# Optimization experiments

Hardware: AMD Instinct MI355X
Metric: run time of the kernel (lower is better)

## Reference

```python
import jax, jax.numpy as jnp
import numpy as np

N, E = 20000, 4096
IN_DIM, DET_DIM, HID, OUT = 512, 256, 256, 2
HALF = HID // 2
EPS = 1e-6


def setup_inputs() -> dict:
    key = jax.random.key(0)
    ks = jax.random.split(key, 20)
    g = lambda k, shape, fan_in: jax.random.normal(k, shape, jnp.float32) / np.sqrt(fan_in)
    return {
        "x": jax.random.normal(ks[0], (N, IN_DIM), jnp.float32),
        "z": jax.random.normal(ks[1], (N, DET_DIM), jnp.float32),
        "incidence": jax.random.uniform(ks[2], (N, E), jnp.float32),
        "edge_weights": jax.random.uniform(ks[3], (E,), jnp.float32),
        "psi_w": g(ks[4], (IN_DIM, HALF), IN_DIM), "psi_b": jnp.zeros((HALF,), jnp.float32),
        "phi_w": g(ks[5], (DET_DIM, HALF), DET_DIM), "phi_b": jnp.zeros((HALF,), jnp.float32),
        "g1_w": g(ks[6], (2 * HALF, HID), 2 * HALF), "g1_b": jnp.zeros((HID,), jnp.float32),
        "g2_w": g(ks[7], (HID, HALF), HID), "g2_b": jnp.zeros((HALF,), jnp.float32),
        "th1": g(ks[8], (HALF, HID), HALF), "b1": jnp.zeros((HID,), jnp.float32),
        "th2": g(ks[9], (HID, HID), HID), "b2": jnp.zeros((HID,), jnp.float32),
        "out_w": g(ks[10], (HID, OUT), HID), "out_b": jnp.zeros((OUT,), jnp.float32),
    }


def hconv(X, H, w, theta, bias):
    # HGNN-style message passing: Dv^{-1/2} H W De^{-1} H^T Dv^{-1/2} (X theta) + b
    Xt = X @ theta                              # [N,F]
    De = H.sum(axis=0)                          # [E] edge degree
    Dv = H @ w                                  # [N] weighted node degree
    inv_sqrt_dv = jax.lax.rsqrt(jnp.maximum(Dv, EPS))[:, None]
    He = H.T @ (Xt * inv_sqrt_dv)               # [E,F] gather to hyperedges
    He = He * (w / jnp.maximum(De, EPS))[:, None]
    return (H @ He) * inv_sqrt_dv + bias        # scatter back to nodes


def reference(x, z, incidence, edge_weights,
              psi_w, psi_b, phi_w, phi_b,
              g1_w, g1_b, g2_w, g2_b,
              th1, b1, th2, b2, out_w, out_b):
    proj_x = x @ psi_w + psi_b                  # [N,HALF]
    proj_z = z @ phi_w + phi_b                  # [N,HALF]
    cat = jnp.concatenate([proj_x, proj_z], axis=1)
    gate = jax.nn.sigmoid(jax.nn.relu(cat @ g1_w + g1_b) @ g2_w + g2_b)
    fused = gate * proj_z + (1.0 - gate) * proj_x
    h = jax.nn.relu(hconv(fused, incidence, edge_weights, th1, b1))
    h = jax.nn.relu(hconv(h, incidence, edge_weights, th2, b2))
    logits = h @ out_w + out_b                  # [N,OUT]
    return logits, gate
```

## Files before the change

kernel.cpp:

```cpp
#include <hip/hip_runtime.h>
#include <hip/hip_bf16.h>


typedef __bf16 bf16_t;
typedef __attribute__((ext_vector_type(8))) __bf16 bf16x8;
typedef __attribute__((ext_vector_type(4))) __bf16 bf16x4;
typedef __attribute__((ext_vector_type(4))) float f32x4;

#define NN 20000
#define NE 4096
#define NNP 20480
#define AT_S 16
#define NEB 8
#define NNB 160

__device__ __forceinline__ f32x4 mfma16(bf16x8 a, bf16x8 b, f32x4 c) {
  return __builtin_amdgcn_mfma_f32_16x16x32_bf16(a, b, c, 0, 0, 0);
}

__device__ __forceinline__ void stats_body(int vbx, int vby,
    const float* __restrict__ H, const float* __restrict__ w,
    float* __restrict__ Dvp, float* __restrict__ Dep, bf16_t* __restrict__ Hbp,
    float (*dvl)[17], float (*deP)[512]) {
  int t = threadIdx.x, l = t & 63, wv = t >> 6;
  long e0 = (long)vbx * 512;
  long n0 = (long)vby * 128;
  long pA = ((e0 >> 6) + (l >> 4)) * (long)NNP;
  long pB = pA + 4 * (long)NNP;
  int inner = (l & 15) * 4;
  f32x4 wa = *(const f32x4*)(w + e0 + l * 4);
  f32x4 wb = *(const f32x4*)(w + e0 + 256 + l * 4);
  f32x4 dea; dea[0] = dea[1] = dea[2] = dea[3] = 0.f;
  f32x4 deb; deb[0] = deb[1] = deb[2] = deb[3] = 0.f;
  #pragma unroll 4
  for (int i = 0; i < 32; ++i) {
    long row = n0 + wv * 32 + i;
    float s;
    if (row < NN) {
      f32x4 ua = *(const f32x4*)(H + row * NE + e0 + l * 4);
      f32x4 ub = *(const f32x4*)(H + row * NE + e0 + 256 + l * 4);
      bf16x4 pa, pb;
      #pragma unroll
      for (int j = 0; j < 4; ++j) { pa[j] = (__bf16)ua[j]; pb[j] = (__bf16)ub[j]; }
      *(bf16x4*)(Hbp + (pA + row) * 64 + inner) = pa;
      *(bf16x4*)(Hbp + (pB + row) * 64 + inner) = pb;
      dea += ua; deb += ub;
      s = ua[0]*wa[0] + ua[1]*wa[1] + ua[2]*wa[2] + ua[3]*wa[3]
        + ub[0]*wb[0] + ub[1]*wb[1] + ub[2]*wb[2] + ub[3]*wb[3];
    } else {
      bf16x4 z;
      #pragma unroll
      for (int j = 0; j < 4; ++j) z[j] = (__bf16)0.f;
      *(bf16x4*)(Hbp + (pA + row) * 64 + inner) = z;
      *(bf16x4*)(Hbp + (pB + row) * 64 + inner) = z;
      s = 0.f;
    }
    s += __shfl_xor(s, 1);
    s += __shfl_xor(s, 2);
    if ((l & 3) == 0) dvl[wv * 32 + i][l >> 2] = s;
  }
  *(f32x4*)(&deP[wv][l * 4]) = dea;
  *(f32x4*)(&deP[wv][256 + l * 4]) = deb;
  __syncthreads();
  if (t < 128) {
    float s = 0.f;
    #pragma unroll
    for (int j = 0; j < 16; ++j) s += dvl[t][j];
    Dvp[(long)vbx * NNP + n0 + t] = s;
  }
  {
    float s0 = deP[0][t] + deP[1][t] + deP[2][t] + deP[3][t];
    float s1 = deP[0][256 + t] + deP[1][256 + t] + deP[2][256 + t] + deP[3][256 + t];
    Dep[(long)vby * NE + e0 + t] = s0;
    Dep[(long)vby * NE + e0 + 256 + t] = s1;
  }
}

__device__ __forceinline__ void cat_gemm_body(const float* __restrict__ Av, int lda,
    const bf16_t* __restrict__ Bt, int K, const float* __restrict__ bias,
    bf16_t* __restrict__ dst, int vbx) {
  int tid = threadIdx.x, l = tid & 63, wv = tid >> 6;
  int lr = l & 15, lq = l >> 4;
  int mo = vbx * 32 + (wv >> 1) * 16;
  int no = (wv & 1) * 64;
  f32x4 acc[4] = {};
  for (int k0 = 0; k0 < K; k0 += 32) {
    int row = mo + lr;
    bf16x8 a;
    if (row < NN) {
      const float* ap = Av + (long)row * lda + k0 + lq * 8;
      f32x4 u0 = *(const f32x4*)ap, u1 = *(const f32x4*)(ap + 4);
      #pragma unroll
      for (int j = 0; j < 4; ++j) { a[j] = (__bf16)u0[j]; a[j + 4] = (__bf16)u1[j]; }
    } else {
      #pragma unroll
      for (int j = 0; j < 8; ++j) a[j] = (__bf16)0.f;
    }
    #pragma unroll
    for (int ni = 0; ni < 4; ++ni) {
      bf16x8 b = *(const bf16x8*)(Bt + (long)(no + ni * 16 + lr) * K + k0 + lq * 8);
      acc[ni] = mfma16(a, b, acc[ni]);
    }
  }
  #pragma unroll
  for (int ni = 0; ni < 4; ++ni) {
    int colf = no + ni * 16 + lr;
    int rb = mo + lq * 4;
    float bs = bias[colf];
    #pragma unroll
    for (int r = 0; r < 4; ++r) {
      int n = rb + r;
      if (n < NN) dst[(long)n * 256 + colf] = (__bf16)(acc[ni][r] + bs);
    }
  }
}

__global__ __launch_bounds__(256) void fusedA_kern(const float* __restrict__ H,
    const float* __restrict__ w, float* __restrict__ Dvp, float* __restrict__ Dep,
    bf16_t* __restrict__ Hbp,
    const float* __restrict__ x, const bf16_t* __restrict__ psi_wt,
    const float* __restrict__ psi_b,
    const float* __restrict__ z, const bf16_t* __restrict__ phi_wt,
    const float* __restrict__ phi_b, bf16_t* __restrict__ cat) {
  __shared__ float dvl[128][17];
  __shared__ float deP[4][512];
  int bid = blockIdx.x;
  if (bid < 1280) {
    stats_body(bid & 7, bid >> 3, H, w, Dvp, Dep, Hbp, dvl, deP);
  } else if (bid < 1905) {
    cat_gemm_body(x, 512, psi_wt, 512, psi_b, cat, bid - 1280);
  } else {
    cat_gemm_body(z, 256, phi_wt, 256, phi_b, cat + 128, bid - 1905);
  }
}

__global__ __launch_bounds__(256) void fusedB_kern(const float* __restrict__ Dvp,
    const float* __restrict__ Dep, const float* __restrict__ w,
    float* __restrict__ isd, float* __restrict__ es,
    const bf16_t* __restrict__ cat, const bf16_t* __restrict__ g1w,
    const float* __restrict__ g1b, bf16_t* __restrict__ hid1) {
  int bid = blockIdx.x;
  if (bid < 79) {
    int t = bid * 256 + threadIdx.x;
    if (t < NN) {
      float s = 0.f;
      #pragma unroll
      for (int b = 0; b < NEB; ++b) s += Dvp[(long)b * NNP + t];
      isd[t] = rsqrtf(fmaxf(s, 1e-6f));
    }
    if (t < NE) {
      float s = 0.f;
      #pragma unroll 8
      for (int b = 0; b < NNB; ++b) s += Dep[(long)b * NE + t];
      es[t] = w[t] / fmaxf(s, 1e-6f);
    }
    return;
  }
  int i = bid - 79;
  int vbx = i % 625, vby = i / 625;
  int tid = threadIdx.x, l = tid & 63, wv = tid >> 6;
  int lr = l & 15, lq = l >> 4;
  int mo = vbx * 32 + (wv >> 1) * 16;
  int no = vby * 128 + (wv & 1) * 64;
  f32x4 acc[4] = {};
  for (int k0 = 0; k0 < 256; k0 += 32) {
    int row = mo + lr;
    bf16x8 a;
    if (row < NN) {
      a = *(const bf16x8*)(cat + (long)row * 256 + k0 + lq * 8);
    } else {
      #pragma unroll
      for (int j = 0; j < 8; ++j) a[j] = (__bf16)0.f;
    }
    #pragma unroll
    for (int ni = 0; ni < 4; ++ni) {
      bf16x8 b = *(const bf16x8*)(g1w + (long)(no + ni * 16 + lr) * 256 + k0 + lq * 8);
      acc[ni] = mfma16(a, b, acc[ni]);
    }
  }
  #pragma unroll
  for (int ni = 0; ni < 4; ++ni) {
    int colf = no + ni * 16 + lr;
    int rb = mo + lq * 4;
    float bs = g1b[colf];
    #pragma unroll
    for (int r = 0; r < 4; ++r) {
      int n = rb + r;
      if (n < NN) {
        float xx = acc[ni][r] + bs;
        hid1[(long)n * 256 + colf] = (__bf16)(xx > 0.f ? xx : 0.f);
      }
    }
  }
}

__global__ void cvtw_kern(const float* __restrict__ psi, const float* __restrict__ phi,
                          const float* __restrict__ g1,  const float* __restrict__ g2,
                          const float* __restrict__ th1, const float* __restrict__ th2,
                          bf16_t* dpsi, bf16_t* dphi, bf16_t* dg1, bf16_t* dg2,
                          bf16_t* dth1, bf16_t* dth2) {
  int t = blockIdx.x * 256 + threadIdx.x;
  if (t < 65536) {
    int nc = t >> 9, k = t & 511; dpsi[t] = (__bf16)psi[k * 128 + nc];
  } else if (t < 98304) {
    int i = t - 65536; int nc = i >> 8, k = i & 255; dphi[i] = (__bf16)phi[k * 128 + nc];
  } else if (t < 163840) {
    int i = t - 98304; int nc = i >> 8, k = i & 255; dg1[i] = (__bf16)g1[k * 256 + nc];
  } else if (t < 196608) {
    int i = t - 163840; int nc = i >> 8, k = i & 255; dg2[i] = (__bf16)g2[k * 128 + nc];
  } else if (t < 229376) {
    int i = t - 196608; int nc = i >> 7, k = i & 127; dth1[i] = (__bf16)th1[k * 256 + nc];
  } else if (t < 294912) {
    int i = t - 229376; int nc = i >> 8, k = i & 255; dth2[i] = (__bf16)th2[k * 256 + nc];
  }
}

__global__ __launch_bounds__(256) void gate_y_kern(
    const bf16_t* __restrict__ hid1, const bf16_t* __restrict__ g2w,
    const float* __restrict__ g2b, const bf16_t* __restrict__ cat,
    const bf16_t* __restrict__ th1w, const float* __restrict__ isd,
    float* __restrict__ gate_out, bf16_t* __restrict__ Yf) {
  __shared__ bf16_t fl[32 * 132];
  int t = threadIdx.x, l = t & 63, wv = t >> 6;
  int lr = l & 15, lq = l >> 4;
  if (blockIdx.x >= 625) {
    bf16x8 z;
    #pragma unroll
    for (int j = 0; j < 8; ++j) z[j] = (__bf16)0.f;
    #pragma unroll
    for (int i = 0; i < 4; ++i)
      *(bf16x8*)(Yf + (((long)(wv + i * 4) * 640 + blockIdx.x) * 64 + l) * 8) = z;
    return;
  }
  long n0 = (long)blockIdx.x * 32;
  int hm = wv >> 1, nq = wv & 1;
  int mo = hm * 16, no = nq * 64;
  f32x4 acc[4] = {};
  for (int k0 = 0; k0 < 256; k0 += 32) {
    bf16x8 a = *(const bf16x8*)(hid1 + (n0 + mo + lr) * 256 + k0 + lq * 8);
    #pragma unroll
    for (int ni = 0; ni < 4; ++ni) {
      bf16x8 b = *(const bf16x8*)(g2w + (long)(no + ni * 16 + lr) * 256 + k0 + lq * 8);
      acc[ni] = mfma16(a, b, acc[ni]);
    }
  }
  #pragma unroll
  for (int ni = 0; ni < 4; ++ni) {
    int colf = no + ni * 16 + lr;
    float bs = g2b[colf];
    #pragma unroll
    for (int r = 0; r < 4; ++r) {
      long n = n0 + mo + lq * 4 + r;
      float g = 1.f / (1.f + __expf(-(acc[ni][r] + bs)));
      gate_out[n * 128 + colf] = g;
      float px = (float)cat[n * 256 + colf];
      float pz = (float)cat[n * 256 + 128 + colf];
      fl[(mo + lq * 4 + r) * 132 + colf] = (__bf16)(g * pz + (1.f - g) * px);
    }
  }
  __syncthreads();
  int hm2 = wv >> 1, f128 = (wv & 1) * 128;
  f32x4 acc2[8] = {};
  for (int k0 = 0; k0 < 128; k0 += 32) {
    bf16x8 a = *(const bf16x8*)(fl + (hm2 * 16 + lr) * 132 + k0 + lq * 8);
    #pragma unroll
    for (int ni = 0; ni < 8; ++ni) {
      bf16x8 b = *(const bf16x8*)(th1w + (long)(f128 + ni * 16 + lr) * 128 + k0 + lq * 8);
      acc2[ni] = mfma16(a, b, acc2[ni]);
    }
  }
  int lanep = (hm2 * 2 + (lq >> 1)) * 16 + lr;
  #pragma unroll
  for (int ni = 0; ni < 8; ++ni) {
    int fblk = (f128 >> 4) + ni;
    bf16x4 pk;
    #pragma unroll
    for (int r = 0; r < 4; ++r) {
      long n = n0 + hm2 * 16 + lq * 4 + r;
      pk[r] = (__bf16)(acc2[ni][r] * isd[n]);
    }
    *(bf16x4*)(Yf + (((long)fblk * 640 + blockIdx.x) * 64 + lanep) * 8 + (lq & 1) * 4) = pk;
  }
}

__global__ __launch_bounds__(512) void at_gemm_kern(const bf16_t* __restrict__ Hbp,
                                                    const bf16_t* __restrict__ Yf,
                                                    bf16_t* __restrict__ part) {
  __shared__ bf16_t T[2][128 * 72];
  int t = threadIdx.x, l = t & 63, wv = t >> 6;
  int lr = l & 15, lq = l >> 4;
  int eh = wv >> 2, fq = wv & 3;
  int e0 = blockIdx.x * 128;
  int s0 = blockIdx.y * 20;
  int rp = t >> 4;
  int ck = t & 15;
  f32x4 acc[4][4] = {};
  const bf16_t* src = Hbp + (((long)(e0 >> 6) + (ck >> 3)) * NNP + (long)s0 * 64 + 2 * rp) * 64
                          + (ck & 7) * 8;
  bf16x8 ra = *(const bf16x8*)src;
  bf16x8 rb = *(const bf16x8*)(src + 64);
  {
    #pragma unroll
    for (int j = 0; j < 8; ++j) {
      int jj = (j + ck) & 7;
      int el = ck * 8 + jj;
      unsigned lo = (unsigned)__builtin_bit_cast(unsigned short, (__bf16)ra[jj]);
      unsigned hi = (unsigned)__builtin_bit_cast(unsigned short, (__bf16)rb[jj]);
      *(unsigned*)(&T[0][el * 72 + rp * 2]) = lo | (hi << 16);
    }
    src += 64 * 64;
    ra = *(const bf16x8*)src;
    rb = *(const bf16x8*)(src + 64);
  }
  for (int i = 0; i < 20; ++i) {
    __syncthreads();
    if (i + 1 < 20) {
      int nb = (i + 1) & 1;
      #pragma unroll
      for (int j = 0; j < 8; ++j) {
        int jj = (j + ck) & 7;
        int el = ck * 8 + jj;
        unsigned lo = (unsigned)__builtin_bit_cast(unsigned short, (__bf16)ra[jj]);
        unsigned hi = (unsigned)__builtin_bit_cast(unsigned short, (__bf16)rb[jj]);
        *(unsigned*)(&T[nb][el * 72 + rp * 2]) = lo | (hi << 16);
      }
    }
    if (i + 2 < 20) {
      src += 64 * 64;
      ra = *(const bf16x8*)src;
      rb = *(const bf16x8*)(src + 64);
    }
    int cb = i & 1;
    int s = s0 + i;
    #pragma unroll
    for (int k32 = 0; k32 < 2; ++k32) {
      bf16x8 a[4], b[4];
      #pragma unroll
      for (int ni = 0; ni < 4; ++ni)
        a[ni] = *(const bf16x8*)(&T[cb][(eh * 64 + ni * 16 + lr) * 72 + k32 * 32 + lq * 8]);
      const bf16_t* bp = Yf + ((long)(s * 2 + k32) * 64 + l) * 8;
      #pragma unroll
      for (int ni = 0; ni < 4; ++ni)
        b[ni] = *(const bf16x8*)(bp + (long)(fq * 4 + ni) * 640 * 512);
      #pragma unroll
      for (int ae = 0; ae < 4; ++ae)
        #pragma unroll
        for (int bf = 0; bf < 4; ++bf)
          acc[ae][bf] = mfma16(a[ae], b[bf], acc[ae][bf]);
    }
  }
  bf16_t* pp = part + (long)blockIdx.y * (256 * 4096);
  #pragma unroll
  for (int ae = 0; ae < 4; ++ae) {
    int eblk16 = (e0 >> 4) + eh * 4 + ae;
    #pragma unroll
    for (int bf = 0; bf < 4; ++bf) {
      int fblk = fq * 4 + bf;
      f32x4 v = acc[ae][bf];
      bf16x4 pk;
      for (int r = 0; r < 4; ++r) pk[r] = (__bf16)v[r];
      *(bf16x4*)(pp + (((long)eblk16 * 16 + fblk) * 64 + l) * 4) = pk;
    }
  }
}

__global__ __launch_bounds__(256) void reduce_he(const bf16_t* __restrict__ part,
                                                 const float* __restrict__ es,
                                                 bf16_t* __restrict__ Hef) {
  int u = blockIdx.x * 256 + threadIdx.x;
  int lane = u & 63, tile = u >> 6;
  int fblk = tile & 15, eblk16 = tile >> 4;
  int lr = lane & 15, lq = lane >> 4;
  int e_base = eblk16 * 16 + lq * 4;
  float a0 = 0.f, a1 = 0.f, a2 = 0.f, a3 = 0.f;
  #pragma unroll
  for (int s = 0; s < AT_S; ++s) {
    bf16x4 v = *(const bf16x4*)(part + (long)s * (256 * 4096) + (long)u * 4);
    a0 += (float)v[0]; a1 += (float)v[1]; a2 += (float)v[2]; a3 += (float)v[3];
  }
  f32x4 e4 = *(const f32x4*)(es + e_base);
  bf16x4 pk;
  pk[0] = (__bf16)(a0 * e4[0]); pk[1] = (__bf16)(a1 * e4[1]);
  pk[2] = (__bf16)(a2 * e4[2]); pk[3] = (__bf16)(a3 * e4[3]);
  int eblk32 = eblk16 >> 1;
  int lanep = ((eblk16 & 1) * 2 + (lq >> 1)) * 16 + lr;
  long slot = (((long)fblk * 128 + eblk32) * 64 + lanep) * 8 + (lq & 1) * 4;
  *(bf16x4*)(Hef + slot) = pk;
}

template<int CONV>
__global__ __launch_bounds__(512) void out_gemm_kern(const bf16_t* __restrict__ Hef,
                                                     const bf16_t* __restrict__ Hbp,
                                                     const float* __restrict__ isd,
                                                     const float* __restrict__ bias,
                                                     const bf16_t* __restrict__ th2w,
                                                     bf16_t* __restrict__ Yf,
                                                     const float* __restrict__ ow,
                                                     const float* __restrict__ ob,
                                                     float* __restrict__ out) {
  __shared__ bf16_t lbuf[2][5120];
  __shared__ float lgp[8][80][2];
  __shared__ bf16_t hl[80 * 260];
  int t = threadIdx.x, l = t & 63, wv = t >> 6;
  int lr = l & 15, lq = l >> 4;
  long r0 = (long)blockIdx.x * 80;
  f32x4 acc[5][2] = {};
  int f1 = wv, f2 = 8 + wv;
  bool has2 = wv < 2;
  const bf16_t* asrc1 = Hbp + (r0 + (f1 >> 1) * 16 + lr) * 64 + (f1 & 1) * 32 + lq * 8;
  const bf16_t* asrc2 = Hbp + (r0 + (f2 >> 1) * 16 + lr) * 64 + (f2 & 1) * 32 + lq * 8;
  const bf16_t* bbase = Hef + (long)l * 8;
  bf16x8 rg1 = *(const bf16x8*)asrc1;
  bf16x8 rg2;
  if (has2) rg2 = *(const bf16x8*)asrc2;
  int c = 0;
  for (int s = 0; s < 64; ++s) {
    *(bf16x8*)(&lbuf[c][f1 * 512 + l * 8]) = rg1;
    if (has2) *(bf16x8*)(&lbuf[c][f2 * 512 + l * 8]) = rg2;
    __syncthreads();
    if (s + 1 < 64) {
      rg1 = *(const bf16x8*)(asrc1 + (long)(s + 1) * NNP * 64);
      if (has2) rg2 = *(const bf16x8*)(asrc2 + (long)(s + 1) * NNP * 64);
    }
    #pragma unroll
    for (int k32 = 0; k32 < 2; ++k32) {
      bf16x8 a[5], b[2];
      #pragma unroll
      for (int mi = 0; mi < 5; ++mi)
        a[mi] = *(const bf16x8*)(&lbuf[c][(mi * 2 + k32) * 512 + l * 8]);
      int eblk = s * 2 + k32;
      #pragma unroll
      for (int ni = 0; ni < 2; ++ni)
        b[ni] = *(const bf16x8*)(bbase + ((long)(wv * 2 + ni) * 128 + eblk) * 512);
      #pragma unroll
      for (int mi = 0; mi < 5; ++mi) {
        acc[mi][0] = mfma16(a[mi], b[0], acc[mi][0]);
        acc[mi][1] = mfma16(a[mi], b[1], acc[mi][1]);
      }
    }
    c ^= 1;
  }
  #pragma unroll
  for (int mi = 0; mi < 5; ++mi) {
    long nb = r0 + mi * 16 + lq * 4;
    #pragma unroll
    for (int r = 0; r < 4; ++r) {
      long n = nb + r;
      float sd = (n < NN) ? isd[n] : 0.f;
      float a0 = 0.f, a1 = 0.f;
      #pragma unroll
      for (int ni = 0; ni < 2; ++ni) {
        int f = wv * 32 + ni * 16 + lr;
        float vv = acc[mi][ni][r] * sd + bias[f];
        vv = vv > 0.f ? vv : 0.f;
        if constexpr (CONV == 1) {
          hl[(mi * 16 + lq * 4 + r) * 260 + f] = (__bf16)vv;
        } else {
          a0 += vv * ow[f * 2];
          a1 += vv * ow[f * 2 + 1];
        }
      }
      if constexpr (CONV == 2) {
        #pragma unroll
        for (int m = 1; m < 16; m <<= 1) { a0 += __shfl_xor(a0, m); a1 += __shfl_xor(a1, m); }
        if (lr == 0) {
          int rowl = mi * 16 + lq * 4 + r;
          lgp[wv][rowl][0] = a0;
          lgp[wv][rowl][1] = a1;
        }
      }
    }
  }
  if constexpr (CONV == 1) {
    __syncthreads();
    f32x4 acc2[5][2] = {};
    for (int k0 = 0; k0 < 256; k0 += 32) {
      bf16x8 a_[5], b2[2];
      #pragma unroll
      for (int mi = 0; mi < 5; ++mi)
        a_[mi] = *(const bf16x8*)(hl + (mi * 16 + lr) * 260 + k0 + lq * 8);
      #pragma unroll
      for (int ni = 0; ni < 2; ++ni)
        b2[ni] = *(const bf16x8*)(th2w + (long)(wv * 32 + ni * 16 + lr) * 256 + k0 + lq * 8);
      #pragma unroll
      for (int mi = 0; mi < 5; ++mi) {
        acc2[mi][0] = mfma16(a_[mi], b2[0], acc2[mi][0]);
        acc2[mi][1] = mfma16(a_[mi], b2[1], acc2[mi][1]);
      }
    }
    #pragma unroll
    for (int mi = 0; mi < 5; ++mi) {
      long nbase = r0 + mi * 16;
      long nblk = nbase >> 5;
      int hm16 = (int)((nbase >> 4) & 1);
      int lanep = (hm16 * 2 + (lq >> 1)) * 16 + lr;
      #pragma unroll
      for (int ni = 0; ni < 2; ++ni) {
        int fblk = wv * 2 + ni;
        bf16x4 pk;
        #pragma unroll
        for (int r = 0; r < 4; ++r) {
          long n = nbase + lq * 4 + r;
          float sc = (n < NN) ? isd[n] : 0.f;
          pk[r] = (__bf16)(acc2[mi][ni][r] * sc);
        }
        *(bf16x4*)(Yf + (((long)fblk * 640 + nblk) * 64 + lanep) * 8 + (lq & 1) * 4) = pk;
      }
    }
  } else {
    __syncthreads();
    if (t < 80) {
      float s0 = 0.f, s1 = 0.f;
      #pragma unroll
      for (int wvi = 0; wvi < 8; ++wvi) { s0 += lgp[wvi][t][0]; s1 += lgp[wvi][t][1]; }
      long n = r0 + t;
      if (n < NN) {
        out[n * 2]     = s0 + ob[0];
        out[n * 2 + 1] = s1 + ob[1];
      }
    }
  }
}

extern "C" void kernel_launch(void* const* d_in, const int* in_sizes, int n_in,
                              void* d_out, int out_size, void* d_ws, size_t ws_size,
                              hipStream_t stream) {
  const float* x    = (const float*)d_in[0];
  const float* z    = (const float*)d_in[1];
  const float* H    = (const float*)d_in[2];
  const float* w    = (const float*)d_in[3];
  const float* psi_w = (const float*)d_in[4];
  const float* psi_b = (const float*)d_in[5];
  const float* phi_w = (const float*)d_in[6];
  const float* phi_b = (const float*)d_in[7];
  const float* g1_w  = (const float*)d_in[8];
  const float* g1_b  = (const float*)d_in[9];
  const float* g2_w  = (const float*)d_in[10];
  const float* g2_b  = (const float*)d_in[11];
  const float* th1   = (const float*)d_in[12];
  const float* b1    = (const float*)d_in[13];
  const float* th2   = (const float*)d_in[14];
  const float* b2    = (const float*)d_in[15];
  const float* out_w = (const float*)d_in[16];
  const float* out_b = (const float*)d_in[17];

  float* logits_out = (float*)d_out;
  float* gate_out   = logits_out + (size_t)NN * 2;

  char* p = (char*)d_ws;
  auto alloc = [&](size_t bytes) { char* r = p; p += (bytes + 255) & ~(size_t)255; return r; };
  float* Dvp  = (float*)alloc((size_t)NEB * NNP * 4);
  float* Dep  = (float*)alloc((size_t)NNB * NE * 4);
  float* isd  = (float*)alloc((size_t)NN * 4);
  float* es   = (float*)alloc((size_t)NE * 4);
  bf16_t* cat   = (bf16_t*)alloc((size_t)NN * 256 * 2);
  bf16_t* hid1  = (bf16_t*)alloc((size_t)NN * 256 * 2);
  bf16_t* Yf    = (bf16_t*)alloc((size_t)16 * 640 * 512 * 2);
  bf16_t* Hef   = (bf16_t*)alloc((size_t)16 * 128 * 512 * 2);
  bf16_t* pbuf  = (bf16_t*)alloc((size_t)AT_S * 256 * 4096 * 2);
  bf16_t* Hbp   = (bf16_t*)alloc((size_t)NNP * NE * 2);
  bf16_t* psi_wt = (bf16_t*)alloc(65536 * 2);
  bf16_t* phi_wt = (bf16_t*)alloc(32768 * 2);
  bf16_t* g1_wt  = (bf16_t*)alloc(65536 * 2);
  bf16_t* g2_wt  = (bf16_t*)alloc(32768 * 2);
  bf16_t* th1_wt = (bf16_t*)alloc(32768 * 2);
  bf16_t* th2_wt = (bf16_t*)alloc(65536 * 2);

  cvtw_kern<<<1152, 256, 0, stream>>>(psi_w, phi_w, g1_w, g2_w, th1, th2,
                                      psi_wt, phi_wt, g1_wt, g2_wt, th1_wt, th2_wt);
  fusedA_kern<<<2530, 256, 0, stream>>>(H, w, Dvp, Dep, Hbp,
                                        x, psi_wt, psi_b, z, phi_wt, phi_b, cat);
  fusedB_kern<<<1329, 256, 0, stream>>>(Dvp, Dep, w, isd, es,
                                        cat, g1_wt, g1_b, hid1);
  gate_y_kern<<<640, 256, 0, stream>>>(hid1, g2_wt, g2_b, cat, th1_wt, isd, gate_out, Yf);

  at_gemm_kern<<<dim3(32, AT_S), 512, 0, stream>>>(Hbp, Yf, pbuf);
  reduce_he<<<1024, 256, 0, stream>>>(pbuf, es, Hef);
  out_gemm_kern<1><<<256, 512, 0, stream>>>(Hef, Hbp, isd, b1, th2_wt, Yf,
                                            nullptr, nullptr, nullptr);

  at_gemm_kern<<<dim3(32, AT_S), 512, 0, stream>>>(Hbp, Yf, pbuf);
  reduce_he<<<1024, 256, 0, stream>>>(pbuf, es, Hef);
  out_gemm_kern<2><<<256, 512, 0, stream>>>(Hef, Hbp, isd, b2, nullptr, nullptr,
                                            out_w, out_b, logits_out);

  (void)in_sizes; (void)n_in; (void)out_size; (void)ws_size;
}
```

Before: 507.1 us.

## Repartition incidence stats so each block covers full rows and computes node degrees directly

Each stats block now processes 16 full rows across all 4096 edges instead of a 128x512 tile. The node degree is reduced inside the block and written straight out as its inverse square root, which removes the Dvp partial buffer and its reduction pass in the next kernel. The trade-off is that edge-degree partials grow from 160 to 1280 per edge, so the es reduction in fusedB now reads 1280 rows from only 16 blocks, which makes that serial tail longer.

```diff
diff --git a/kernel.cpp b/kernel.cpp
--- a/kernel.cpp
+++ b/kernel.cpp
@@ -11,68 +11,65 @@
 #define NE 4096
 #define NNP 20480
 #define AT_S 16
-#define NEB 8
-#define NNB 160
+#define DE_PARTS 1280
 
 __device__ __forceinline__ f32x4 mfma16(bf16x8 a, bf16x8 b, f32x4 c) {
   return __builtin_amdgcn_mfma_f32_16x16x32_bf16(a, b, c, 0, 0, 0);
 }
 
-__device__ __forceinline__ void stats_body(int vbx, int vby,
+__device__ __forceinline__ void stats_body(int vby,
     const float* __restrict__ H, const float* __restrict__ w,
-    float* __restrict__ Dvp, float* __restrict__ Dep, bf16_t* __restrict__ Hbp,
-    float (*dvl)[17], float (*deP)[512]) {
+    float* __restrict__ isd, float* __restrict__ Dep, bf16_t* __restrict__ Hbp,
+    float (*dvl)[64]) {
   int t = threadIdx.x, l = t & 63, wv = t >> 6;
-  long e0 = (long)vbx * 512;
-  long n0 = (long)vby * 128;
-  long pA = ((e0 >> 6) + (l >> 4)) * (long)NNP;
-  long pB = pA + 4 * (long)NNP;
-  int inner = (l & 15) * 4;
-  f32x4 wa = *(const f32x4*)(w + e0 + l * 4);
-  f32x4 wb = *(const f32x4*)(w + e0 + 256 + l * 4);
-  f32x4 dea; dea[0] = dea[1] = dea[2] = dea[3] = 0.f;
-  f32x4 deb; deb[0] = deb[1] = deb[2] = deb[3] = 0.f;
-  #pragma unroll 4
-  for (int i = 0; i < 32; ++i) {
-    long row = n0 + wv * 32 + i;
-    float s;
+  long n0 = (long)vby * 16;
+  f32x4 w4[4];
+  #pragma unroll
+  for (int s = 0; s < 4; ++s) w4[s] = *(const f32x4*)(w + s * 1024 + t * 4);
+  f32x4 de[4];
+  #pragma unroll
+  for (int s = 0; s < 4; ++s) { de[s][0] = de[s][1] = de[s][2] = de[s][3] = 0.f; }
+  for (int i = 0; i < 16; ++i) {
+    long row = n0 + i;
+    float sv = 0.f;
     if (row < NN) {
-      f32x4 ua = *(const f32x4*)(H + row * NE + e0 + l * 4);
-      f32x4 ub = *(const f32x4*)(H + row * NE + e0 + 256 + l * 4);
-      bf16x4 pa, pb;
-      #pragma unroll
-      for (int j = 0; j < 4; ++j) { pa[j] = (__bf16)ua[j]; pb[j] = (__bf16)ub[j]; }
-      *(bf16x4*)(Hbp + (pA + row) * 64 + inner) = pa;
-      *(bf16x4*)(Hbp + (pB + row) * 64 + inner) = pb;
-      dea += ua; deb += ub;
-      s = ua[0]*wa[0] + ua[1]*wa[1] + ua[2]*wa[2] + ua[3]*wa[3]
-        + ub[0]*wb[0] + ub[1]*wb[1] + ub[2]*wb[2] + ub[3]*wb[3];
+      #pragma unroll
+      for (int s = 0; s < 4; ++s) {
+        int col = s * 1024 + t * 4;
+        f32x4 u = *(const f32x4*)(H + row * NE + col);
+        bf16x4 pk;
+        #pragma unroll
+        for (int j = 0; j < 4; ++j) pk[j] = (__bf16)u[j];
+        *(bf16x4*)(Hbp + ((long)(col >> 6) * NNP + row) * 64 + (col & 63)) = pk;
+        de[s] += u;
+        sv += u[0]*w4[s][0] + u[1]*w4[s][1] + u[2]*w4[s][2] + u[3]*w4[s][3];
+      }
     } else {
       bf16x4 z;
       #pragma unroll
       for (int j = 0; j < 4; ++j) z[j] = (__bf16)0.f;
-      *(bf16x4*)(Hbp + (pA + row) * 64 + inner) = z;
-      *(bf16x4*)(Hbp + (pB + row) * 64 + inner) = z;
-      s = 0.f;
-    }
-    s += __shfl_xor(s, 1);
-    s += __shfl_xor(s, 2);
-    if ((l & 3) == 0) dvl[wv * 32 + i][l >> 2] = s;
-  }
-  *(f32x4*)(&deP[wv][l * 4]) = dea;
-  *(f32x4*)(&deP[wv][256 + l * 4]) = deb;
+      #pragma unroll
+      for (int s = 0; s < 4; ++s) {
+        int col = s * 1024 + t * 4;
+        *(bf16x4*)(Hbp + ((long)(col >> 6) * NNP + row) * 64 + (col & 63)) = z;
+      }
+    }
+    sv += __shfl_xor(sv, 1);
+    sv += __shfl_xor(sv, 2);
+    if ((l & 3) == 0) dvl[i][wv * 16 + (l >> 2)] = sv;
+  }
+  #pragma unroll
+  for (int s = 0; s < 4; ++s)
+    *(f32x4*)(Dep + (long)vby * NE + s * 1024 + t * 4) = de[s];
   __syncthreads();
-  if (t < 128) {
-    float s = 0.f;
-    #pragma unroll
-    for (int j = 0; j < 16; ++j) s += dvl[t][j];
-    Dvp[(long)vbx * NNP + n0 + t] = s;
-  }
   {
-    float s0 = deP[0][t] + deP[1][t] + deP[2][t] + deP[3][t];
-    float s1 = deP[0][256 + t] + deP[1][256 + t] + deP[2][256 + t] + deP[3][256 + t];
-    Dep[(long)vby * NE + e0 + t] = s0;
-    Dep[(long)vby * NE + e0 + 256 + t] = s1;
+    int row_i = t >> 4, k = t & 15;
+    float s = dvl[row_i][k * 4] + dvl[row_i][k * 4 + 1]
+            + dvl[row_i][k * 4 + 2] + dvl[row_i][k * 4 + 3];
+    #pragma unroll
+    for (int m = 1; m < 16; m <<= 1) s += __shfl_xor(s, m);
+    long row = n0 + row_i;
+    if (k == 0 && row < NN) isd[row] = rsqrtf(fmaxf(s, 1e-6f));
   }
 }
 
@@ -116,17 +113,16 @@
 }
 
 __global__ __launch_bounds__(256) void fusedA_kern(const float* __restrict__ H,
-    const float* __restrict__ w, float* __restrict__ Dvp, float* __restrict__ Dep,
+    const float* __restrict__ w, float* __restrict__ isd, float* __restrict__ Dep,
     bf16_t* __restrict__ Hbp,
     const float* __restrict__ x, const bf16_t* __restrict__ psi_wt,
     const float* __restrict__ psi_b,
     const float* __restrict__ z, const bf16_t* __restrict__ phi_wt,
     const float* __restrict__ phi_b, bf16_t* __restrict__ cat) {
-  __shared__ float dvl[128][17];
-  __shared__ float deP[4][512];
+  __shared__ float dvl[16][64];
   int bid = blockIdx.x;
   if (bid < 1280) {
-    stats_body(bid & 7, bid >> 3, H, w, Dvp, Dep, Hbp, dvl, deP);
+    stats_body(bid, H, w, isd, Dep, Hbp, dvl);
   } else if (bid < 1905) {
     cat_gemm_body(x, 512, psi_wt, 512, psi_b, cat, bid - 1280);
   } else {
@@ -134,29 +130,20 @@
   }
 }
 
-__global__ __launch_bounds__(256) void fusedB_kern(const float* __restrict__ Dvp,
-    const float* __restrict__ Dep, const float* __restrict__ w,
-    float* __restrict__ isd, float* __restrict__ es,
+__global__ __launch_bounds__(256) void fusedB_kern(const float* __restrict__ Dep,
+    const float* __restrict__ w, float* __restrict__ es,
     const bf16_t* __restrict__ cat, const bf16_t* __restrict__ g1w,
     const float* __restrict__ g1b, bf16_t* __restrict__ hid1) {
   int bid = blockIdx.x;
-  if (bid < 79) {
-    int t = bid * 256 + threadIdx.x;
-    if (t < NN) {
-      float s = 0.f;
-      #pragma unroll
-      for (int b = 0; b < NEB; ++b) s += Dvp[(long)b * NNP + t];
-      isd[t] = rsqrtf(fmaxf(s, 1e-6f));
-    }
-    if (t < NE) {
-      float s = 0.f;
-      #pragma unroll 8
-      for (int b = 0; b < NNB; ++b) s += Dep[(long)b * NE + t];
-      es[t] = w[t] / fmaxf(s, 1e-6f);
-    }
+  if (bid < 16) {
+    int e = bid * 256 + threadIdx.x;
+    float s = 0.f;
+    #pragma unroll 8
+    for (int b = 0; b < DE_PARTS; ++b) s += Dep[(long)b * NE + e];
+    es[e] = w[e] / fmaxf(s, 1e-6f);
     return;
   }
-  int i = bid - 79;
+  int i = bid - 16;
   int vbx = i % 625, vby = i / 625;
   int tid = threadIdx.x, l = tid & 63, wv = tid >> 6;
   int lr = l & 15, lq = l >> 4;
@@ -549,8 +536,7 @@
 
   char* p = (char*)d_ws;
   auto alloc = [&](size_t bytes) { char* r = p; p += (bytes + 255) & ~(size_t)255; return r; };
-  float* Dvp  = (float*)alloc((size_t)NEB * NNP * 4);
-  float* Dep  = (float*)alloc((size_t)NNB * NE * 4);
+  float* Dep  = (float*)alloc((size_t)DE_PARTS * NE * 4);
   float* isd  = (float*)alloc((size_t)NN * 4);
   float* es   = (float*)alloc((size_t)NE * 4);
   bf16_t* cat   = (bf16_t*)alloc((size_t)NN * 256 * 2);
@@ -568,10 +554,9 @@
 
   cvtw_kern<<<1152, 256, 0, stream>>>(psi_w, phi_w, g1_w, g2_w, th1, th2,
                                       psi_wt, phi_wt, g1_wt, g2_wt, th1_wt, th2_wt);
-  fusedA_kern<<<2530, 256, 0, stream>>>(H, w, Dvp, Dep, Hbp,
+  fusedA_kern<<<2530, 256, 0, stream>>>(H, w, isd, Dep, Hbp,
                                         x, psi_wt, psi_b, z, phi_wt, phi_b, cat);
-  fusedB_kern<<<1329, 256, 0, stream>>>(Dvp, Dep, w, isd, es,
-                                        cat, g1_wt, g1_b, hid1);
+  fusedB_kern<<<1266, 256, 0, stream>>>(Dep, w, es, cat, g1_wt, g1_b, hid1);
   gate_y_kern<<<640, 256, 0, stream>>>(hid1, g2_wt, g2_b, cat, th1_wt, isd, gate_out, Yf);
 
   at_gemm_kern<<<dim3(32, AT_S), 512, 0, stream>>>(Hbp, Yf, pbuf);
```

Result: slower. 540.1 us (+6.5%).
